# Kernel tuning notes

Measured on AMD Instinct MI355X. Metric: run time of the kernel, lower is better.

Reference implementation:

```python
import jax, jax.numpy as jnp
import numpy as np

I, O, R = 64, 64, 896          # input / output / regulatory protein counts
N = I + O + R                  # total GRN size
WARMUP = 25                    # warmup_count


def setup_inputs() -> dict:
    key = jax.random.key(0)
    k1, k2, k3, k4 = jax.random.split(key, 4)
    return {
        "inputs": jax.random.uniform(k1, (16384, I), dtype=jnp.float32),
        "identifiers": jax.random.uniform(k2, (N,), dtype=jnp.float32),
        "enhancers": jax.random.uniform(k3, (N,), dtype=jnp.float32),
        "inhibitors": jax.random.uniform(k4, (N,), dtype=jnp.float32),
        "beta": jnp.full((1,), 2.0, dtype=jnp.float32),
        "delta": jnp.full((1,), 1.0, dtype=jnp.float32),
    }


def _signatures(identifiers, enhancers, inhibitors, beta):
    # sig[j, i] = exp(-beta * |tag_j - id_i|): affinity of protein j regulating protein i.
    enh = jnp.exp(-beta * jnp.abs(enhancers[:, None] - identifiers[None, :]))
    inh = jnp.exp(-beta * jnp.abs(inhibitors[:, None] - identifiers[None, :]))
    # output proteins do not regulate others -> zero their rows
    mask = jnp.ones((N,), dtype=enh.dtype).at[I:I + O].set(0.0)[:, None]
    return enh * mask, inh * mask


def _step(conc, sig_diff, delta):
    # conc: [..., N]; sig_diff = enh_sigs - inh_sigs: [N, N]
    dc = (delta / N) * (conc @ sig_diff)
    new = jnp.maximum(conc + dc, 0.0)
    reg = new[..., I:]                                    # outputs + regulatory
    s = jnp.sum(reg, axis=-1, keepdims=True)
    reg = jnp.where(s > 0, reg / s, reg)                  # renormalize
    return jnp.concatenate([conc[..., :I], reg], axis=-1)  # inputs clamped


def reference(inputs, identifiers, enhancers, inhibitors, beta, delta):
    b, d = beta[0], delta[0]
    enh_s, inh_s = _signatures(identifiers, enhancers, inhibitors, b)
    sig_diff = enh_s - inh_s

    # setup(): uniform initial concentrations; warmup(): shared sequential steps
    conc0 = jnp.full((N,), 1.0 / N, dtype=jnp.float32)
    def warm(c, _):
        return _step(c, sig_diff, d), None
    conc, _ = jax.lax.scan(warm, conc0, None, length=WARMUP)

    # per-sample (batched instead of tf.map_fn): set input concs, one step
    B = inputs.shape[0]
    batch_conc = jnp.concatenate(
        [inputs, jnp.broadcast_to(conc[I:], (B, N - I))], axis=-1)
    new = _step(batch_conc, sig_diff, d)
    return new[..., I:I + O]  # output protein concentrations [B, O]
```

## Files before the change

### kernel.cpp

```cpp
#include <hip/hip_runtime.h>
#include <math.h>

#define NJ 960
#define NSRC 896
#define NWARM 25

typedef unsigned long long u64;
typedef unsigned int u32;

#define RK_O 0u
#define CT_O 896u
#define HD_O 1856u
#define BSP_O 2816u
#define DN_O 3776u

#define TAG_RK 0x524B0001u
#define TAG_CT 0x43540001u
#define TAG_HD 0x48440001u
#define TAG_DN 0x444E0001u

__device__ __forceinline__ void ast(u64* p, u64 v) {
  __hip_atomic_store(p, v, __ATOMIC_RELAXED, __HIP_MEMORY_SCOPE_AGENT);
}
__device__ __forceinline__ u64 ald(const u64* p) {
  return __hip_atomic_load(p, __ATOMIC_RELAXED, __HIP_MEMORY_SCOPE_AGENT);
}
__device__ __forceinline__ u32 poll32(const u64* p, u32 tag) {
  u64 v = ald(p);
  while ((u32)(v >> 32) != tag) { __builtin_amdgcn_s_sleep(1); v = ald(p); }
  return (u32)v;
}

struct ScanSm {
  float yl[NJ];
  float2 scanE[1024];
  float2 scanI[1024];
  float4 wtot[4];
  float ssw[4];
};
struct BatSm {
  float At[64][16];
  float Wl[16][520];
  float bch[NJ];
  float4 Ek4[64];
  float2 Ei2[64];
};

__global__ __launch_bounds__(256, 2) void grn_all(
    const float* __restrict__ inp, const float* __restrict__ ident,
    const float* __restrict__ enh, const float* __restrict__ inh,
    const float* __restrict__ beta, const float* __restrict__ delta,
    void* __restrict__ wsv, float* __restrict__ out) {
  __shared__ __align__(16) char smraw[(sizeof(BatSm) > sizeof(ScanSm))
                                          ? sizeof(BatSm) : sizeof(ScanSm)];
  u64* RK = (u64*)wsv + RK_O;
  u64* CT = (u64*)wsv + CT_O;
  u64* HD = (u64*)wsv + HD_O;
  u64* BSP = (u64*)wsv + BSP_O;
  u64* DN = (u64*)wsv + DN_O;

  const int tid = threadIdx.x;
  const float bb = beta[0];
  const float dN = delta[0] / 1024.0f;

  if (blockIdx.x == 0) {
    ScanSm& S = *(ScanSm*)smraw;
    const int lane = tid & 63, wvid = tid >> 6;

    int rE[4], rI[4];
    if (tid < 224) {
      #pragma unroll
      for (int s = 0; s < 4; ++s) {
        u32 v = poll32(&RK[4 * tid + s], TAG_RK);
        rE[s] = v & 0xFFFF; rI[s] = v >> 16;
      }
    }
    int cE[4], cI[4];
    float hd[4], fm[4], fp[4];
    if (tid < 240) {
      #pragma unroll
      for (int c = 0; c < 4; ++c) {
        u32 v = poll32(&CT[4 * tid + c], TAG_CT);
        cE[c] = v & 0xFFFF; cI[c] = v >> 16;
        hd[c] = __uint_as_float(poll32(&HD[4 * tid + c], TAG_HD));
        float cj = ident[64 + 4 * tid + c];
        fm[c] = expf(-bb * cj); fp[c] = expf(bb * cj);
      }
    }
    float EP[4], EN[4], IP[4], IN2[4];
    if (tid < 224) {
      #pragma unroll
      for (int s = 0; s < 4; ++s) {
        float e = enh[128 + 4 * tid + s], i2 = inh[128 + 4 * tid + s];
        EP[s] = expf(bb * e);  EN[s] = expf(-bb * e);
        IP[s] = expf(bb * i2); IN2[s] = expf(-bb * i2);
      }
    }
    float y_own[4] = {1.0f / 1024.0f, 1.0f / 1024.0f, 1.0f / 1024.0f, 1.0f / 1024.0f};
    if (tid < 240) {
      #pragma unroll
      for (int c = 0; c < 4; ++c) S.yl[4 * tid + c] = 1.0f / 1024.0f;
    }
    __syncthreads();

    for (int t = 0; t <= NWARM; ++t) {
      if (tid == 0) {
        S.scanE[0] = make_float2(0.f, 0.f);
        S.scanI[0] = make_float2(0.f, 0.f);
      }
      if (tid >= 224) {
        #pragma unroll
        for (int c = 0; c < 4; ++c) {
          int p = 4 * tid + c;
          if (p > NSRC) {
            S.scanE[p] = make_float2(0.f, 0.f);
            S.scanI[p] = make_float2(0.f, 0.f);
          }
        }
      }
      if (tid < 224) {
        #pragma unroll
        for (int s = 0; s < 4; ++s) {
          float ym = S.yl[64 + 4 * tid + s];
          S.scanE[rE[s] + 1] = make_float2(ym * EP[s], ym * EN[s]);
          S.scanI[rI[s] + 1] = make_float2(ym * IP[s], ym * IN2[s]);
        }
      }
      __syncthreads();

      float2 e0 = S.scanE[4 * tid], e1 = S.scanE[4 * tid + 1],
             e2 = S.scanE[4 * tid + 2], e3 = S.scanE[4 * tid + 3];
      float2 i0 = S.scanI[4 * tid], i1 = S.scanI[4 * tid + 1],
             i2v = S.scanI[4 * tid + 2], i3 = S.scanI[4 * tid + 3];
      e1.x += e0.x; e1.y += e0.y; e2.x += e1.x; e2.y += e1.y; e3.x += e2.x; e3.y += e2.y;
      i1.x += i0.x; i1.y += i0.y; i2v.x += i1.x; i2v.y += i1.y; i3.x += i2v.x; i3.y += i2v.y;
      float4 tot = make_float4(e3.x, e3.y, i3.x, i3.y);
      float4 inc = tot;
      #pragma unroll
      for (int off = 1; off < 64; off <<= 1) {
        float ox = __shfl_up(inc.x, off, 64);
        float oy = __shfl_up(inc.y, off, 64);
        float oz = __shfl_up(inc.z, off, 64);
        float ow = __shfl_up(inc.w, off, 64);
        if (lane >= off) { inc.x += ox; inc.y += oy; inc.z += oz; inc.w += ow; }
      }
      if (lane == 63) S.wtot[wvid] = inc;
      __syncthreads();
      float4 exc = make_float4(inc.x - tot.x, inc.y - tot.y,
                               inc.z - tot.z, inc.w - tot.w);
      #pragma unroll
      for (int w = 0; w < 3; ++w)
        if (w < wvid) {
          float4 p = S.wtot[w];
          exc.x += p.x; exc.y += p.y; exc.z += p.z; exc.w += p.w;
        }
      e0.x += exc.x; e0.y += exc.y; e1.x += exc.x; e1.y += exc.y;
      e2.x += exc.x; e2.y += exc.y; e3.x += exc.x; e3.y += exc.y;
      i0.x += exc.z; i0.y += exc.w; i1.x += exc.z; i1.y += exc.w;
      i2v.x += exc.z; i2v.y += exc.w; i3.x += exc.z; i3.y += exc.w;
      S.scanE[4 * tid] = e0; S.scanE[4 * tid + 1] = e1;
      S.scanE[4 * tid + 2] = e2; S.scanE[4 * tid + 3] = e3;
      S.scanI[4 * tid] = i0; S.scanI[4 * tid + 1] = i1;
      S.scanI[4 * tid + 2] = i2v; S.scanI[4 * tid + 3] = i3;
      __syncthreads();

      float nv[4] = {0.f, 0.f, 0.f, 0.f};
      float psum = 0.0f;
      if (tid < 240) {
        float2 TE = S.scanE[NSRC], TI = S.scanI[NSRC];
        float pr[4];
        #pragma unroll
        for (int c = 0; c < 4; ++c) {
          float2 AE = S.scanE[cE[c]], AI = S.scanI[cI[c]];
          float dot = fm[c] * AE.x + fp[c] * (TE.y - AE.y)
                    - fm[c] * AI.x - fp[c] * (TI.y - AI.y);
          float pre = y_own[c] + dN * dot;
          pr[c] = pre;
          if (t < NWARM) {
            nv[c] = fmaxf(pre + hd[c], 0.0f);
            psum += nv[c];
          }
        }
        if (t == NWARM) {
          ast(&BSP[2 * tid],
              (u64)__float_as_uint(pr[0]) | ((u64)__float_as_uint(pr[1]) << 32));
          ast(&BSP[2 * tid + 1],
              (u64)__float_as_uint(pr[2]) | ((u64)__float_as_uint(pr[3]) << 32));
        }
      }
      if (t < NWARM) {
        #pragma unroll
        for (int off = 32; off >= 1; off >>= 1) psum += __shfl_xor(psum, off);
        if (lane == 0) S.ssw[wvid] = psum;
        __syncthreads();
        float s2 = S.ssw[0] + S.ssw[1] + S.ssw[2] + S.ssw[3];
        float inv = (s2 > 0.0f) ? 1.0f / s2 : 1.0f;
        if (tid < 240) {
          #pragma unroll
          for (int c = 0; c < 4; ++c) {
            y_own[c] = nv[c] * inv;
            S.yl[4 * tid + c] = y_own[c];
          }
        }
      }
      __syncthreads();
    }
    if (tid == 0)
      __hip_atomic_store(DN, ((u64)TAG_DN << 32) | 1u, __ATOMIC_RELEASE,
                         __HIP_MEMORY_SCOPE_AGENT);
    return;
  }

  if (blockIdx.x <= 30) {
    const int g = (int)(blockIdx.x - 1) * 256 + tid;
    const int c8 = g & 7;
    if (g < NSRC * 8) {
      int m = g >> 3;
      float myE = enh[128 + m], myI = inh[128 + m];
      int re = 0, ri = 0;
      for (int i = 112 * c8; i < 112 * c8 + 112; ++i) {
        float ev = enh[128 + i], iv = inh[128 + i];
        re += (ev < myE || (ev == myE && i < m)) ? 1 : 0;
        ri += (iv < myI || (iv == myI && i < m)) ? 1 : 0;
      }
      int p = re | (ri << 16);
      p += __shfl_xor(p, 1); p += __shfl_xor(p, 2); p += __shfl_xor(p, 4);
      if (c8 == 0) ast(&RK[m], ((u64)TAG_RK << 32) | (u32)p);
    }
    {
      int j = g >> 3;
      float cj = ident[64 + j];
      int ce = 0, ci = 0;
      for (int i = 112 * c8; i < 112 * c8 + 112; ++i) {
        ce += (enh[128 + i] <= cj) ? 1 : 0;
        ci += (inh[128 + i] <= cj) ? 1 : 0;
      }
      int p = ce | (ci << 16);
      p += __shfl_xor(p, 1); p += __shfl_xor(p, 2); p += __shfl_xor(p, 4);
      if (c8 == 0) ast(&CT[j], ((u64)TAG_CT << 32) | (u32)p);
    }
    {
      int j = g >> 3;
      float cj = ident[64 + j];
      float h = 0.0f;
      for (int k = 8 * c8; k < 8 * c8 + 8; ++k)
        h += expf(-bb * fabsf(enh[k] - cj)) - expf(-bb * fabsf(inh[k] - cj));
      h += __shfl_xor(h, 1); h += __shfl_xor(h, 2); h += __shfl_xor(h, 4);
      if (c8 == 0)
        ast(&HD[j], ((u64)TAG_HD << 32) |
                    (u64)__float_as_uint(dN * h * (1.0f / 1024.0f)));
    }
  }

  BatSm& Bm = *(BatSm*)smraw;
  const int colg = tid & 63;
  const int rowg = tid >> 6;
  const size_t rowbase = (size_t)(blockIdx.x - 1) * 16;

  {
    int r = tid >> 4, c4 = (tid & 15) * 4;
    float4 f4 = *(const float4*)(inp + (rowbase + r) * 64 + c4);
    Bm.At[c4 + 0][r] = f4.x; Bm.At[c4 + 1][r] = f4.y;
    Bm.At[c4 + 2][r] = f4.z; Bm.At[c4 + 3][r] = f4.w;
  }
  if (tid < 64) {
    float e = enh[tid], iv = inh[tid];
    Bm.Ek4[tid] = make_float4(expf(bb * e), expf(-bb * e),
                              expf(bb * iv), expf(-bb * iv));
    Bm.Ei2[tid] = make_float2(e, iv);
  }

  float acc0[4][8], acc1[4][8];
  #pragma unroll
  for (int r = 0; r < 4; ++r)
    #pragma unroll
    for (int c = 0; c < 8; ++c) { acc0[r][c] = 0.0f; acc1[r][c] = 0.0f; }


  {
    const float cjA = ident[64 + tid];
    const float cjB = ident[64 + 256 + tid];
    const float fpA = expf(bb * cjA), fmA = expf(-bb * cjA);
    const float fpB = expf(bb * cjB), fmB = expf(-bb * cjB);
    #pragma unroll 1
    for (int s = 0; s < 4; ++s) {
      __syncthreads();
      #pragma unroll 4
      for (int e = 0; e < 16; ++e) {
        int k = 16 * s + e;
        float4 E = Bm.Ek4[k];
        float2 ei = Bm.Ei2[k];
        Bm.Wl[e][tid] = dN * (((ei.x >= cjA) ? E.y * fpA : E.x * fmA)
                            - ((ei.y >= cjA) ? E.w * fpA : E.z * fmA));
        Bm.Wl[e][tid + 256] = dN * (((ei.x >= cjB) ? E.y * fpB : E.x * fmB)
                                  - ((ei.y >= cjB) ? E.w * fpB : E.z * fmB));
      }
      __syncthreads();
      #pragma unroll
      for (int kk = 0; kk < 16; ++kk) {
        float4 av = *(const float4*)&Bm.At[16 * s + kk][rowg * 4];
        float4 w0 = *(const float4*)&Bm.Wl[kk][colg * 4];
        float4 w1 = *(const float4*)&Bm.Wl[kk][256 + colg * 4];
        float a_[4] = {av.x, av.y, av.z, av.w};
        float w_[8] = {w0.x, w0.y, w0.z, w0.w, w1.x, w1.y, w1.z, w1.w};
        #pragma unroll
        for (int r = 0; r < 4; ++r)
          #pragma unroll
          for (int c = 0; c < 8; ++c)
            acc0[r][c] = fmaf(a_[r], w_[c], acc0[r][c]);
      }
    }
  }

  {
    const float cjA = ident[64 + 512 + tid];
    const bool okB = (768 + tid) < NJ;
    const float cjB = okB ? ident[64 + 768 + tid] : 0.0f;
    const float fpA = expf(bb * cjA), fmA = expf(-bb * cjA);
    const float fpB = expf(bb * cjB), fmB = expf(-bb * cjB);
    #pragma unroll 1
    for (int s = 0; s < 4; ++s) {
      __syncthreads();
      #pragma unroll 4
      for (int e = 0; e < 16; ++e) {
        int k = 16 * s + e;
        float4 E = Bm.Ek4[k];
        float2 ei = Bm.Ei2[k];
        Bm.Wl[e][tid] = dN * (((ei.x >= cjA) ? E.y * fpA : E.x * fmA)
                            - ((ei.y >= cjA) ? E.w * fpA : E.z * fmA));
        float wB = 0.0f;
        if (okB)
          wB = dN * (((ei.x >= cjB) ? E.y * fpB : E.x * fmB)
                   - ((ei.y >= cjB) ? E.w * fpB : E.z * fmB));
        Bm.Wl[e][tid + 256] = wB;
      }
      __syncthreads();
      #pragma unroll
      for (int kk = 0; kk < 16; ++kk) {
        float4 av = *(const float4*)&Bm.At[16 * s + kk][rowg * 4];
        float4 w0 = *(const float4*)&Bm.Wl[kk][colg * 4];
        float4 w1 = *(const float4*)&Bm.Wl[kk][256 + colg * 4];
        float a_[4] = {av.x, av.y, av.z, av.w};
        float w_[8] = {w0.x, w0.y, w0.z, w0.w, w1.x, w1.y, w1.z, w1.w};
        #pragma unroll
        for (int r = 0; r < 4; ++r)
          #pragma unroll
          for (int c = 0; c < 8; ++c)
            acc1[r][c] = fmaf(a_[r], w_[c], acc1[r][c]);
      }
    }
  }

  if (tid == 0) {
    u64 v = ald(DN);
    while ((u32)(v >> 32) != TAG_DN) { __builtin_amdgcn_s_sleep(32); v = ald(DN); }
    (void)__hip_atomic_load(DN, __ATOMIC_ACQUIRE, __HIP_MEMORY_SCOPE_AGENT);
  }
  __syncthreads();
  if (tid < 240) {
    u64 w0 = ald(&BSP[2 * tid]);
    u64 w1 = ald(&BSP[2 * tid + 1]);
    Bm.bch[4 * tid + 0] = __uint_as_float((u32)w0);
    Bm.bch[4 * tid + 1] = __uint_as_float((u32)(w0 >> 32));
    Bm.bch[4 * tid + 2] = __uint_as_float((u32)w1);
    Bm.bch[4 * tid + 3] = __uint_as_float((u32)(w1 >> 32));
  }
  __syncthreads();

  float rs[4] = {0.f, 0.f, 0.f, 0.f};
  #pragma unroll
  for (int c = 0; c < 8; ++c) {
    int cl = (c < 4) ? (colg * 4 + c) : (256 + colg * 4 + (c - 4));
    float bv0 = Bm.bch[cl];
    int j1 = 512 + cl;
    float bv1 = (j1 < NJ) ? Bm.bch[j1] : -1.0e30f;
    #pragma unroll
    for (int r = 0; r < 4; ++r) {
      rs[r] += fmaxf(acc0[r][c] + bv0, 0.0f);
      rs[r] += fmaxf(acc1[r][c] + bv1, 0.0f);
    }
  }
  #pragma unroll
  for (int r = 0; r < 4; ++r) {
    float v = rs[r];
    #pragma unroll
    for (int off = 32; off >= 1; off >>= 1) v += __shfl_xor(v, off);
    rs[r] = v;
  }
  if (colg < 16) {
    #pragma unroll
    for (int r = 0; r < 4; ++r) {
      float inv = (rs[r] > 0.0f) ? 1.0f / rs[r] : 1.0f;
      float* op = out + (rowbase + rowg * 4 + r) * 64 + colg * 4;
      float4 o;
      o.x = fmaxf(acc0[r][0] + Bm.bch[colg * 4 + 0], 0.0f) * inv;
      o.y = fmaxf(acc0[r][1] + Bm.bch[colg * 4 + 1], 0.0f) * inv;
      o.z = fmaxf(acc0[r][2] + Bm.bch[colg * 4 + 2], 0.0f) * inv;
      o.w = fmaxf(acc0[r][3] + Bm.bch[colg * 4 + 3], 0.0f) * inv;
      *(float4*)op = o;
    }
  }
}

extern "C" void kernel_launch(void* const* d_in, const int* in_sizes, int n_in,
                              void* d_out, int out_size, void* d_ws, size_t ws_size,
                              hipStream_t stream) {
  const float* inp   = (const float*)d_in[0];
  const float* ident = (const float*)d_in[1];
  const float* enh   = (const float*)d_in[2];
  const float* inh   = (const float*)d_in[3];
  const float* beta  = (const float*)d_in[4];
  const float* delta = (const float*)d_in[5];

  hipLaunchKernelGGL(grn_all, dim3(1025), dim3(256), 0, stream,
                     inp, ident, enh, inh, beta, delta, d_ws, (float*)d_out);
}
```

Measured before the change: 171.7 us.

## Alias weight and bias smem, hoist loads, shrink grid, stagger block starts

Puts the Wl weight tile and the bch bias buffer in a union to cut shared memory per block, and hoists the input, tag and identifier global loads to the top of the kernel so they overlap the setup work. The grid shrinks from 1025 to 1024 blocks, with block 1 processing the final tile in a second pass so the batch fits one wave. Non-setup blocks sleep for a staggered interval, apparently to leave the serial warmup block and the precompute blocks more issue bandwidth. The sleeps add idle time to the batch blocks, and block 1 now does twice the work of the others.

```diff
diff --git a/kernel.cpp b/kernel.cpp
--- a/kernel.cpp
+++ b/kernel.cpp
@@ -40,8 +40,10 @@
 };
 struct BatSm {
   float At[64][16];
-  float Wl[16][520];
-  float bch[NJ];
+  union {
+    float Wl[16][512];
+    float bch[NJ];
+  };
   float4 Ek4[64];
   float2 Ei2[64];
 };
@@ -211,6 +213,17 @@
     return;
   }
 
+  const int r_ld = tid >> 4, c4_ld = (tid & 15) * 4;
+  float4 f4 = *(const float4*)(inp + ((size_t)(blockIdx.x - 1) * 16 + r_ld) * 64 + c4_ld);
+  float eL = 0.f, ivL = 0.f;
+  if (tid < 64) { eL = enh[tid]; ivL = inh[tid]; }
+  const float cjA0 = ident[64 + tid];
+  const float cjB0 = ident[64 + 256 + tid];
+  const float cjA1 = ident[64 + 512 + tid];
+  const bool okB1 = (768 + tid) < NJ;
+  const float cjB1 = okB1 ? ident[64 + 768 + tid] : 0.0f;
+  asm volatile("" :: "v"(f4.x), "v"(f4.y), "v"(f4.z), "v"(f4.w));
+
   if (blockIdx.x <= 30) {
     const int g = (int)(blockIdx.x - 1) * 256 + tid;
     const int c8 = g & 7;
@@ -250,154 +263,153 @@
         ast(&HD[j], ((u64)TAG_HD << 32) |
                     (u64)__float_as_uint(dN * h * (1.0f / 1024.0f)));
     }
+  } else {
+    const int nsleep = 4 + (int)(blockIdx.x & 7);
+    for (int i = 0; i < nsleep; ++i) __builtin_amdgcn_s_sleep(127);
   }
 
   BatSm& Bm = *(BatSm*)smraw;
   const int colg = tid & 63;
   const int rowg = tid >> 6;
-  const size_t rowbase = (size_t)(blockIdx.x - 1) * 16;
-
-  {
-    int r = tid >> 4, c4 = (tid & 15) * 4;
-    float4 f4 = *(const float4*)(inp + (rowbase + r) * 64 + c4);
-    Bm.At[c4 + 0][r] = f4.x; Bm.At[c4 + 1][r] = f4.y;
-    Bm.At[c4 + 2][r] = f4.z; Bm.At[c4 + 3][r] = f4.w;
-  }
-  if (tid < 64) {
-    float e = enh[tid], iv = inh[tid];
-    Bm.Ek4[tid] = make_float4(expf(bb * e), expf(-bb * e),
-                              expf(bb * iv), expf(-bb * iv));
-    Bm.Ei2[tid] = make_float2(e, iv);
-  }
-
-  float acc0[4][8], acc1[4][8];
-  #pragma unroll
-  for (int r = 0; r < 4; ++r)
+  const int nsub = (blockIdx.x == 1) ? 2 : 1;
+
+  const float fpA0 = expf(bb * cjA0), fmA0 = expf(-bb * cjA0);
+  const float fpB0 = expf(bb * cjB0), fmB0 = expf(-bb * cjB0);
+  const float fpA1 = expf(bb * cjA1), fmA1 = expf(-bb * cjA1);
+  const float fpB1 = expf(bb * cjB1), fmB1 = expf(-bb * cjB1);
+
+  for (int sub = 0; sub < nsub; ++sub) {
+    const int tile = (sub == 0) ? (int)blockIdx.x - 1 : 1023;
+    const size_t rowbase = (size_t)tile * 16;
+    if (sub == 1)
+      f4 = *(const float4*)(inp + (rowbase + r_ld) * 64 + c4_ld);
+
+    Bm.At[c4_ld + 0][r_ld] = f4.x; Bm.At[c4_ld + 1][r_ld] = f4.y;
+    Bm.At[c4_ld + 2][r_ld] = f4.z; Bm.At[c4_ld + 3][r_ld] = f4.w;
+    if (sub == 0 && tid < 64) {
+      Bm.Ek4[tid] = make_float4(expf(bb * eL), expf(-bb * eL),
+                                expf(bb * ivL), expf(-bb * ivL));
+      Bm.Ei2[tid] = make_float2(eL, ivL);
+    }
+
+    float acc0[4][8], acc1[4][8];
     #pragma unroll
-    for (int c = 0; c < 8; ++c) { acc0[r][c] = 0.0f; acc1[r][c] = 0.0f; }
-
-
-  {
-    const float cjA = ident[64 + tid];
-    const float cjB = ident[64 + 256 + tid];
-    const float fpA = expf(bb * cjA), fmA = expf(-bb * cjA);
-    const float fpB = expf(bb * cjB), fmB = expf(-bb * cjB);
-    #pragma unroll 1
-    for (int s = 0; s < 4; ++s) {
-      __syncthreads();
-      #pragma unroll 4
-      for (int e = 0; e < 16; ++e) {
-        int k = 16 * s + e;
-        float4 E = Bm.Ek4[k];
-        float2 ei = Bm.Ei2[k];
-        Bm.Wl[e][tid] = dN * (((ei.x >= cjA) ? E.y * fpA : E.x * fmA)
-                            - ((ei.y >= cjA) ? E.w * fpA : E.z * fmA));
-        Bm.Wl[e][tid + 256] = dN * (((ei.x >= cjB) ? E.y * fpB : E.x * fmB)
-                                  - ((ei.y >= cjB) ? E.w * fpB : E.z * fmB));
-      }
-      __syncthreads();
-      #pragma unroll
-      for (int kk = 0; kk < 16; ++kk) {
-        float4 av = *(const float4*)&Bm.At[16 * s + kk][rowg * 4];
-        float4 w0 = *(const float4*)&Bm.Wl[kk][colg * 4];
-        float4 w1 = *(const float4*)&Bm.Wl[kk][256 + colg * 4];
-        float a_[4] = {av.x, av.y, av.z, av.w};
-        float w_[8] = {w0.x, w0.y, w0.z, w0.w, w1.x, w1.y, w1.z, w1.w};
-        #pragma unroll
-        for (int r = 0; r < 4; ++r)
+    for (int r = 0; r < 4; ++r)
+      #pragma unroll
+      for (int c = 0; c < 8; ++c) { acc0[r][c] = 0.0f; acc1[r][c] = 0.0f; }
+
+    {
+      #pragma unroll 1
+      for (int s = 0; s < 4; ++s) {
+        __syncthreads();
+        #pragma unroll 4
+        for (int e = 0; e < 16; ++e) {
+          int k = 16 * s + e;
+          float4 E = Bm.Ek4[k];
+          float2 ei = Bm.Ei2[k];
+          Bm.Wl[e][tid] = dN * (((ei.x >= cjA0) ? E.y * fpA0 : E.x * fmA0)
+                              - ((ei.y >= cjA0) ? E.w * fpA0 : E.z * fmA0));
+          Bm.Wl[e][tid + 256] = dN * (((ei.x >= cjB0) ? E.y * fpB0 : E.x * fmB0)
+                                    - ((ei.y >= cjB0) ? E.w * fpB0 : E.z * fmB0));
+        }
+        __syncthreads();
+        #pragma unroll
+        for (int kk = 0; kk < 16; ++kk) {
+          float4 av = *(const float4*)&Bm.At[16 * s + kk][rowg * 4];
+          float4 w0 = *(const float4*)&Bm.Wl[kk][colg * 4];
+          float4 w1 = *(const float4*)&Bm.Wl[kk][256 + colg * 4];
+          float a_[4] = {av.x, av.y, av.z, av.w};
+          float w_[8] = {w0.x, w0.y, w0.z, w0.w, w1.x, w1.y, w1.z, w1.w};
           #pragma unroll
-          for (int c = 0; c < 8; ++c)
-            acc0[r][c] = fmaf(a_[r], w_[c], acc0[r][c]);
-      }
-    }
-  }
-
-  {
-    const float cjA = ident[64 + 512 + tid];
-    const bool okB = (768 + tid) < NJ;
-    const float cjB = okB ? ident[64 + 768 + tid] : 0.0f;
-    const float fpA = expf(bb * cjA), fmA = expf(-bb * cjA);
-    const float fpB = expf(bb * cjB), fmB = expf(-bb * cjB);
-    #pragma unroll 1
-    for (int s = 0; s < 4; ++s) {
-      __syncthreads();
-      #pragma unroll 4
-      for (int e = 0; e < 16; ++e) {
-        int k = 16 * s + e;
-        float4 E = Bm.Ek4[k];
-        float2 ei = Bm.Ei2[k];
-        Bm.Wl[e][tid] = dN * (((ei.x >= cjA) ? E.y * fpA : E.x * fmA)
-                            - ((ei.y >= cjA) ? E.w * fpA : E.z * fmA));
-        float wB = 0.0f;
-        if (okB)
-          wB = dN * (((ei.x >= cjB) ? E.y * fpB : E.x * fmB)
-                   - ((ei.y >= cjB) ? E.w * fpB : E.z * fmB));
-        Bm.Wl[e][tid + 256] = wB;
-      }
-      __syncthreads();
-      #pragma unroll
-      for (int kk = 0; kk < 16; ++kk) {
-        float4 av = *(const float4*)&Bm.At[16 * s + kk][rowg * 4];
-        float4 w0 = *(const float4*)&Bm.Wl[kk][colg * 4];
-        float4 w1 = *(const float4*)&Bm.Wl[kk][256 + colg * 4];
-        float a_[4] = {av.x, av.y, av.z, av.w};
-        float w_[8] = {w0.x, w0.y, w0.z, w0.w, w1.x, w1.y, w1.z, w1.w};
-        #pragma unroll
-        for (int r = 0; r < 4; ++r)
+          for (int r = 0; r < 4; ++r)
+            #pragma unroll
+            for (int c = 0; c < 8; ++c)
+              acc0[r][c] = fmaf(a_[r], w_[c], acc0[r][c]);
+        }
+      }
+    }
+    {
+      #pragma unroll 1
+      for (int s = 0; s < 4; ++s) {
+        __syncthreads();
+        #pragma unroll 4
+        for (int e = 0; e < 16; ++e) {
+          int k = 16 * s + e;
+          float4 E = Bm.Ek4[k];
+          float2 ei = Bm.Ei2[k];
+          Bm.Wl[e][tid] = dN * (((ei.x >= cjA1) ? E.y * fpA1 : E.x * fmA1)
+                              - ((ei.y >= cjA1) ? E.w * fpA1 : E.z * fmA1));
+          float wB = 0.0f;
+          if (okB1)
+            wB = dN * (((ei.x >= cjB1) ? E.y * fpB1 : E.x * fmB1)
+                     - ((ei.y >= cjB1) ? E.w * fpB1 : E.z * fmB1));
+          Bm.Wl[e][tid + 256] = wB;
+        }
+        __syncthreads();
+        #pragma unroll
+        for (int kk = 0; kk < 16; ++kk) {
+          float4 av = *(const float4*)&Bm.At[16 * s + kk][rowg * 4];
+          float4 w0 = *(const float4*)&Bm.Wl[kk][colg * 4];
+          float4 w1 = *(const float4*)&Bm.Wl[kk][256 + colg * 4];
+          float a_[4] = {av.x, av.y, av.z, av.w};
+          float w_[8] = {w0.x, w0.y, w0.z, w0.w, w1.x, w1.y, w1.z, w1.w};
           #pragma unroll
-          for (int c = 0; c < 8; ++c)
-            acc1[r][c] = fmaf(a_[r], w_[c], acc1[r][c]);
-      }
-    }
-  }
-
-  if (tid == 0) {
-    u64 v = ald(DN);
-    while ((u32)(v >> 32) != TAG_DN) { __builtin_amdgcn_s_sleep(32); v = ald(DN); }
-    (void)__hip_atomic_load(DN, __ATOMIC_ACQUIRE, __HIP_MEMORY_SCOPE_AGENT);
-  }
-  __syncthreads();
-  if (tid < 240) {
-    u64 w0 = ald(&BSP[2 * tid]);
-    u64 w1 = ald(&BSP[2 * tid + 1]);
-    Bm.bch[4 * tid + 0] = __uint_as_float((u32)w0);
-    Bm.bch[4 * tid + 1] = __uint_as_float((u32)(w0 >> 32));
-    Bm.bch[4 * tid + 2] = __uint_as_float((u32)w1);
-    Bm.bch[4 * tid + 3] = __uint_as_float((u32)(w1 >> 32));
-  }
-  __syncthreads();
-
-  float rs[4] = {0.f, 0.f, 0.f, 0.f};
-  #pragma unroll
-  for (int c = 0; c < 8; ++c) {
-    int cl = (c < 4) ? (colg * 4 + c) : (256 + colg * 4 + (c - 4));
-    float bv0 = Bm.bch[cl];
-    int j1 = 512 + cl;
-    float bv1 = (j1 < NJ) ? Bm.bch[j1] : -1.0e30f;
+          for (int r = 0; r < 4; ++r)
+            #pragma unroll
+            for (int c = 0; c < 8; ++c)
+              acc1[r][c] = fmaf(a_[r], w_[c], acc1[r][c]);
+        }
+      }
+    }
+
+    if (tid == 0) {
+      u64 v = ald(DN);
+      while ((u32)(v >> 32) != TAG_DN) { __builtin_amdgcn_s_sleep(32); v = ald(DN); }
+      (void)__hip_atomic_load(DN, __ATOMIC_ACQUIRE, __HIP_MEMORY_SCOPE_AGENT);
+    }
+    __syncthreads();
+    if (tid < 240) {
+      u64 w0 = ald(&BSP[2 * tid]);
+      u64 w1 = ald(&BSP[2 * tid + 1]);
+      Bm.bch[4 * tid + 0] = __uint_as_float((u32)w0);
+      Bm.bch[4 * tid + 1] = __uint_as_float((u32)(w0 >> 32));
+      Bm.bch[4 * tid + 2] = __uint_as_float((u32)w1);
+      Bm.bch[4 * tid + 3] = __uint_as_float((u32)(w1 >> 32));
+    }
+    __syncthreads();
+
+    float rs[4] = {0.f, 0.f, 0.f, 0.f};
+    #pragma unroll
+    for (int c = 0; c < 8; ++c) {
+      int cl = (c < 4) ? (colg * 4 + c) : (256 + colg * 4 + (c - 4));
+      float bv0 = Bm.bch[cl];
+      int j1 = 512 + cl;
+      float bv1 = (j1 < NJ) ? Bm.bch[j1] : -1.0e30f;
+      #pragma unroll
+      for (int r = 0; r < 4; ++r) {
+        rs[r] += fmaxf(acc0[r][c] + bv0, 0.0f);
+        rs[r] += fmaxf(acc1[r][c] + bv1, 0.0f);
+      }
+    }
     #pragma unroll
     for (int r = 0; r < 4; ++r) {
-      rs[r] += fmaxf(acc0[r][c] + bv0, 0.0f);
-      rs[r] += fmaxf(acc1[r][c] + bv1, 0.0f);
-    }
-  }
-  #pragma unroll
-  for (int r = 0; r < 4; ++r) {
-    float v = rs[r];
-    #pragma unroll
-    for (int off = 32; off >= 1; off >>= 1) v += __shfl_xor(v, off);
-    rs[r] = v;
-  }
-  if (colg < 16) {
-    #pragma unroll
-    for (int r = 0; r < 4; ++r) {
-      float inv = (rs[r] > 0.0f) ? 1.0f / rs[r] : 1.0f;
-      float* op = out + (rowbase + rowg * 4 + r) * 64 + colg * 4;
-      float4 o;
-      o.x = fmaxf(acc0[r][0] + Bm.bch[colg * 4 + 0], 0.0f) * inv;
-      o.y = fmaxf(acc0[r][1] + Bm.bch[colg * 4 + 1], 0.0f) * inv;
-      o.z = fmaxf(acc0[r][2] + Bm.bch[colg * 4 + 2], 0.0f) * inv;
-      o.w = fmaxf(acc0[r][3] + Bm.bch[colg * 4 + 3], 0.0f) * inv;
-      *(float4*)op = o;
+      float v = rs[r];
+      #pragma unroll
+      for (int off = 32; off >= 1; off >>= 1) v += __shfl_xor(v, off);
+      rs[r] = v;
+    }
+    if (colg < 16) {
+      #pragma unroll
+      for (int r = 0; r < 4; ++r) {
+        float inv = (rs[r] > 0.0f) ? 1.0f / rs[r] : 1.0f;
+        float* op = out + (rowbase + rowg * 4 + r) * 64 + colg * 4;
+        float4 o;
+        o.x = fmaxf(acc0[r][0] + Bm.bch[colg * 4 + 0], 0.0f) * inv;
+        o.y = fmaxf(acc0[r][1] + Bm.bch[colg * 4 + 1], 0.0f) * inv;
+        o.z = fmaxf(acc0[r][2] + Bm.bch[colg * 4 + 2], 0.0f) * inv;
+        o.w = fmaxf(acc0[r][3] + Bm.bch[colg * 4 + 3], 0.0f) * inv;
+        *(float4*)op = o;
+      }
     }
   }
 }
@@ -412,6 +424,6 @@
   const float* beta  = (const float*)d_in[4];
   const float* delta = (const float*)d_in[5];
 
-  hipLaunchKernelGGL(grn_all, dim3(1025), dim3(256), 0, stream,
+  hipLaunchKernelGGL(grn_all, dim3(1024), dim3(256), 0, stream,
                      inp, ident, enh, inh, beta, delta, d_ws, (float*)d_out);
 }
```

Result: slower. 199.3 us (+16.1%).
